# Performance work log

Hardware: AMD Instinct MI355X
Metric: run time of the kernel (lower is better)

## Reference

```python
import jax, jax.numpy as jnp
import numpy as np

EPS = 1e-7  # K.epsilon()
ROUTINGS = 3
NUM_CAPSULE = 8
FILTERS = 16


def squash(v, axis=-1):
    s2 = jnp.sum(jnp.square(v), axis=axis, keepdims=True)
    scale = s2 / (1.0 + s2) / jnp.sqrt(s2 + EPS)
    return scale * v


def _conv_per_caps(x, w):
    # x: [B,H,W,Cin], w: [k,k,Cin,Cout]
    return jax.lax.conv_general_dilated(
        x, w, window_strides=(1, 1), padding='SAME',
        dimension_numbers=('NHWC', 'HWIO', 'NHWC'))


def setup_inputs() -> dict:
    key = jax.random.key(0)
    k1, k2 = jax.random.split(key, 2)
    B, H, Wd, IN_CAPS, IN_F = 32, 32, 32, 8, 16
    input_tensor = jax.random.normal(k1, (B, H, Wd, IN_CAPS, IN_F), dtype=jnp.float32)
    # he_normal fan_in = k*k*Cin = 3*3*16 = 144
    W = jax.random.normal(k2, (IN_CAPS, 3, 3, IN_F, NUM_CAPSULE * FILTERS), dtype=jnp.float32) * np.sqrt(2.0 / 144.0)
    b = jnp.full((1, 1, NUM_CAPSULE, FILTERS), 0.1, dtype=jnp.float32)
    return {"input_tensor": input_tensor, "W": W, "b": b}


def reference(input_tensor, W, b):
    B, H, Wd, in_caps, in_f = input_tensor.shape
    # per-input-capsule conv: vmap over capsule axis of input and weight
    votes = jax.vmap(_conv_per_caps, in_axes=(3, 0), out_axes=1)(input_tensor, W)
    # [B, in_caps, H, W, num_cap*F] -> [B, in_caps, H, W, num_cap, F]
    votes = votes.reshape(B, in_caps, H, Wd, NUM_CAPSULE, FILTERS)

    # dynamic routing
    logits = jnp.zeros((B, in_caps, H, Wd, NUM_CAPSULE), dtype=votes.dtype)
    activation = None
    for i in range(ROUTINGS):
        route = jax.nn.softmax(logits, axis=-1)  # over output capsules
        # sum over input capsules of route-weighted votes, plus bias
        preactivate = jnp.einsum('bihwc,bihwcf->bhwcf', route, votes) + b
        activation = squash(preactivate, axis=-1)
        if i < ROUTINGS - 1:
            # scalar-product agreement
            logits = logits + jnp.einsum('bihwcf,bhwcf->bihwc', votes, activation)
    return activation.astype(jnp.float32)
```

## Files before the change

### kernel.cpp

```cpp
#include <hip/hip_runtime.h>
#include <math.h>


typedef _Float16 fp16x8 __attribute__((ext_vector_type(8)));
typedef float f32x4 __attribute__((ext_vector_type(4)));

#define EPS 1e-7f
constexpr int PSTRIDE = 136;
constexpr int LSTRIDE = 76;
constexpr int PXS     = 76;
constexpr int W_ELEMS = 40 * 8 * 64 * 8;

template<int CTRL>
__device__ __forceinline__ float dpp_rot(float v) {
    int s = __float_as_int(v);
    return __int_as_float(__builtin_amdgcn_update_dpp(s, s, CTRL, 0xF, 0xF, false));
}
__device__ __forceinline__ float sum16(float v) {
    v += dpp_rot<0x128>(v);
    v += dpp_rot<0x124>(v);
    v += dpp_rot<0x122>(v);
    v += dpp_rot<0x121>(v);
    return v;
}

__global__ __launch_bounds__(256)
void prep_weights(const float* __restrict__ wts,
                  _Float16* __restrict__ w16) {
    int n = blockIdx.x * 256 + threadIdx.x;
    if (n >= W_ELEMS) return;
    int j    = n & 7;
    int ln   = (n >> 3) & 63;
    int c0   = (n >> 9) & 7;
    int iq   = n >> 12;
    int i0   = iq / 5;
    int q0   = iq - i0 * 5;
    int quad0 = ln >> 4, fi0 = ln & 15;
    int k = q0 * 32 + quad0 * 8 + j;
    float w = 0.f;
    if (k < 144) w = wts[(i0 * 144 + k) * 128 + c0 * 16 + fi0];
    w16[n] = (_Float16)w;
}

__global__ __launch_bounds__(1024, 8)
void capsule_mfma_kernel(const float* __restrict__ x,
                         const _Float16* __restrict__ w16,
                         const float* __restrict__ bias,
                         float* __restrict__ out)
{
    __shared__ _Float16 patch[3 * 34 * PSTRIDE];
    __shared__ float lg_arr[32 * LSTRIDE];
    __shared__ float r_arr[32 * PXS];

    const int tid  = threadIdx.x;
    const int lane = tid & 63;
    const int wv   = tid >> 6;
    const int c    = wv & 7;
    const int Mt   = wv >> 3;
    const int fi   = lane & 15;
    const int quad = lane >> 4;
    const int lane8 = lane * 8;

    const int bid = blockIdx.x;
    const int h = bid & 31, b = bid >> 5;

    const float4* x4 = (const float4*)x;
    for (int idx = tid; idx < 102 * 32; idx += 1024) {
        int ch4  = idx & 31;
        int slot = idx >> 5;
        int row  = slot / 34;
        int colp = slot - row * 34;
        int gh = h - 1 + row;
        int gw = colp - 1;
        float4 v = {0.f, 0.f, 0.f, 0.f};
        if ((unsigned)gh < 32u && (unsigned)gw < 32u)
            v = x4[(((b * 32 + gh) * 32 + gw) << 5) + ch4];
        _Float16 ph[4];
        ph[0] = (_Float16)v.x; ph[1] = (_Float16)v.y;
        ph[2] = (_Float16)v.z; ph[3] = (_Float16)v.w;
        *(ushort4*)&patch[slot * PSTRIDE + ch4 * 4] = *(const ushort4*)ph;
    }
    __syncthreads();

    int a_off[5];
    #pragma unroll
    for (int q = 0; q < 5; ++q) {
        int tap = 2 * q + (quad >> 1);
        if (tap > 8) tap = 8;
        int dy = tap / 3, dx = tap - dy * 3;
        a_off[q] = (dy * 34 + (Mt * 16 + fi + dx)) * PSTRIDE + (quad & 1) * 8;
    }

    f32x4 acc[8];
    #pragma unroll
    for (int i = 0; i < 8; ++i) acc[i] = (f32x4){0.f, 0.f, 0.f, 0.f};

    #pragma unroll
    for (int q = 0; q < 5; ++q) {
        #pragma unroll
        for (int i = 0; i < 8; ++i) {
            int boff = ((i * 5 + q) * 8 + c) * 512 + lane8;
            fp16x8 bh = *(const fp16x8*)(w16 + boff);
            fp16x8 ah = *(const fp16x8*)(patch + a_off[q] + i * 16);
            acc[i] = __builtin_amdgcn_mfma_f32_16x16x32_f16(ah, bh, acc[i], 0, 0, 0);
        }
    }

    const float bb  = bias[c * 16 + fi];
    const int   px0 = Mt * 16 + quad * 4;
    float act[4];

    #pragma unroll
    for (int r = 0; r < 4; ++r) {
        float s = 0.f;
        #pragma unroll
        for (int i = 0; i < 8; ++i) s += acc[i][r];
        float pre = s * 0.125f + bb;
        float s2 = sum16(pre * pre);
        float scale = s2 * __builtin_amdgcn_rsqf(s2 + EPS) * __builtin_amdgcn_rcpf(1.f + s2);
        act[r] = scale * pre;
    }
    #pragma unroll
    for (int i = 0; i < 8; ++i)
        #pragma unroll
        for (int r = 0; r < 4; ++r) {
            float a = sum16(acc[i][r] * act[r]);
            if (fi == 0) lg_arr[(px0 + r) * LSTRIDE + i * 9 + c] = a;
        }
    __syncthreads();
    if (tid < 256) {
        int p = tid >> 3, ii = tid & 7;
        const float* lrow = &lg_arr[p * LSTRIDE + ii * 9];
        float m = lrow[0];
        #pragma unroll
        for (int cc = 1; cc < 8; ++cc) m = fmaxf(m, lrow[cc]);
        float e[8]; float den = 0.f;
        #pragma unroll
        for (int cc = 0; cc < 8; ++cc) { e[cc] = __expf(lrow[cc] - m); den += e[cc]; }
        float rd = __builtin_amdgcn_rcpf(den);
        #pragma unroll
        for (int cc = 0; cc < 8; ++cc) r_arr[p * PXS + cc * 8 + ii] = e[cc] * rd;
    }
    __syncthreads();

    #pragma unroll
    for (int r = 0; r < 4; ++r) {
        const float4* rp = (const float4*)&r_arr[(px0 + r) * PXS + c * 8];
        float4 r0 = rp[0], r1 = rp[1];
        float s;
        s  = r0.x * acc[0][r]; s = fmaf(r0.y, acc[1][r], s);
        s  = fmaf(r0.z, acc[2][r], s); s = fmaf(r0.w, acc[3][r], s);
        s  = fmaf(r1.x, acc[4][r], s); s = fmaf(r1.y, acc[5][r], s);
        s  = fmaf(r1.z, acc[6][r], s); s = fmaf(r1.w, acc[7][r], s);
        float pre = s + bb;
        float s2 = sum16(pre * pre);
        float scale = s2 * __builtin_amdgcn_rsqf(s2 + EPS) * __builtin_amdgcn_rcpf(1.f + s2);
        act[r] = scale * pre;
    }
    #pragma unroll
    for (int i = 0; i < 8; ++i)
        #pragma unroll
        for (int r = 0; r < 4; ++r) {
            float a = sum16(acc[i][r] * act[r]);
            if (fi == 0) lg_arr[(px0 + r) * LSTRIDE + i * 9 + c] += a;
        }
    __syncthreads();
    if (tid < 256) {
        int p = tid >> 3, ii = tid & 7;
        const float* lrow = &lg_arr[p * LSTRIDE + ii * 9];
        float m = lrow[0];
        #pragma unroll
        for (int cc = 1; cc < 8; ++cc) m = fmaxf(m, lrow[cc]);
        float e[8]; float den = 0.f;
        #pragma unroll
        for (int cc = 0; cc < 8; ++cc) { e[cc] = __expf(lrow[cc] - m); den += e[cc]; }
        float rd = __builtin_amdgcn_rcpf(den);
        #pragma unroll
        for (int cc = 0; cc < 8; ++cc) r_arr[p * PXS + cc * 8 + ii] = e[cc] * rd;
    }
    __syncthreads();

    #pragma unroll
    for (int r = 0; r < 4; ++r) {
        const float4* rp = (const float4*)&r_arr[(px0 + r) * PXS + c * 8];
        float4 r0 = rp[0], r1 = rp[1];
        float s;
        s  = r0.x * acc[0][r]; s = fmaf(r0.y, acc[1][r], s);
        s  = fmaf(r0.z, acc[2][r], s); s = fmaf(r0.w, acc[3][r], s);
        s  = fmaf(r1.x, acc[4][r], s); s = fmaf(r1.y, acc[5][r], s);
        s  = fmaf(r1.z, acc[6][r], s); s = fmaf(r1.w, acc[7][r], s);
        float pre = s + bb;
        float s2 = sum16(pre * pre);
        float scale = s2 * __builtin_amdgcn_rsqf(s2 + EPS) * __builtin_amdgcn_rcpf(1.f + s2);
        int px = px0 + r;
        out[(((b * 32 + h) * 32 + px) << 7) + c * 16 + fi] = scale * pre;
    }
}

extern "C" void kernel_launch(void* const* d_in, const int* in_sizes, int n_in,
                              void* d_out, int out_size, void* d_ws, size_t ws_size,
                              hipStream_t stream) {
    const float* x    = (const float*)d_in[0];
    const float* wts  = (const float*)d_in[1];
    const float* bias = (const float*)d_in[2];
    float* out        = (float*)d_out;
    _Float16* w16     = (_Float16*)d_ws;

    prep_weights<<<dim3(640), dim3(256), 0, stream>>>(wts, w16);
    capsule_mfma_kernel<<<dim3(1024), dim3(1024), 0, stream>>>(x, w16, bias, out);
}
```

Baseline: 118.2 us.

## Swap MFMA operands, drop weight prep kernel, use quad-shuffle reductions

Removes the separate fp16 weight-repacking launch and has each wave load fp32 weights straight from global memory, converting them to fp16 in registers. The weights become the A operand and the input patch the B operand, so each lane holds one pixel with four filter values. The 16-lane DPP reductions become two cross-quad shuffles, and output stores widen to float4. In exchange, every block does strided scalar global weight loads and conversions (8 loads per MFMA) instead of one contiguous 16-byte load.

```diff
diff --git a/kernel.cpp b/kernel.cpp
--- a/kernel.cpp
+++ b/kernel.cpp
@@ -9,42 +9,16 @@
 constexpr int PSTRIDE = 136;
 constexpr int LSTRIDE = 76;
 constexpr int PXS     = 76;
-constexpr int W_ELEMS = 40 * 8 * 64 * 8;
 
-template<int CTRL>
-__device__ __forceinline__ float dpp_rot(float v) {
-    int s = __float_as_int(v);
-    return __int_as_float(__builtin_amdgcn_update_dpp(s, s, CTRL, 0xF, 0xF, false));
-}
-__device__ __forceinline__ float sum16(float v) {
-    v += dpp_rot<0x128>(v);
-    v += dpp_rot<0x124>(v);
-    v += dpp_rot<0x122>(v);
-    v += dpp_rot<0x121>(v);
+__device__ __forceinline__ float sumquad(float v) {
+    v += __shfl_xor(v, 16);
+    v += __shfl_xor(v, 32);
     return v;
-}
-
-__global__ __launch_bounds__(256)
-void prep_weights(const float* __restrict__ wts,
-                  _Float16* __restrict__ w16) {
-    int n = blockIdx.x * 256 + threadIdx.x;
-    if (n >= W_ELEMS) return;
-    int j    = n & 7;
-    int ln   = (n >> 3) & 63;
-    int c0   = (n >> 9) & 7;
-    int iq   = n >> 12;
-    int i0   = iq / 5;
-    int q0   = iq - i0 * 5;
-    int quad0 = ln >> 4, fi0 = ln & 15;
-    int k = q0 * 32 + quad0 * 8 + j;
-    float w = 0.f;
-    if (k < 144) w = wts[(i0 * 144 + k) * 128 + c0 * 16 + fi0];
-    w16[n] = (_Float16)w;
 }
 
 __global__ __launch_bounds__(1024, 8)
 void capsule_mfma_kernel(const float* __restrict__ x,
-                         const _Float16* __restrict__ w16,
+                         const float* __restrict__ wts,
                          const float* __restrict__ bias,
                          float* __restrict__ out)
 {
@@ -57,9 +31,8 @@
     const int wv   = tid >> 6;
     const int c    = wv & 7;
     const int Mt   = wv >> 3;
-    const int fi   = lane & 15;
+    const int l15  = lane & 15;
     const int quad = lane >> 4;
-    const int lane8 = lane * 8;
 
     const int bid = blockIdx.x;
     const int h = bid & 31, b = bid >> 5;
@@ -88,45 +61,57 @@
         int tap = 2 * q + (quad >> 1);
         if (tap > 8) tap = 8;
         int dy = tap / 3, dx = tap - dy * 3;
-        a_off[q] = (dy * 34 + (Mt * 16 + fi + dx)) * PSTRIDE + (quad & 1) * 8;
+        a_off[q] = (dy * 34 + (Mt * 16 + l15 + dx)) * PSTRIDE + (quad & 1) * 8;
     }
 
     f32x4 acc[8];
     #pragma unroll
     for (int i = 0; i < 8; ++i) acc[i] = (f32x4){0.f, 0.f, 0.f, 0.f};
 
+    const float* wl = wts + quad * 8 * 128 + c * 16 + l15;
     #pragma unroll
     for (int q = 0; q < 5; ++q) {
         #pragma unroll
         for (int i = 0; i < 8; ++i) {
-            int boff = ((i * 5 + q) * 8 + c) * 512 + lane8;
-            fp16x8 bh = *(const fp16x8*)(w16 + boff);
-            fp16x8 ah = *(const fp16x8*)(patch + a_off[q] + i * 16);
-            acc[i] = __builtin_amdgcn_mfma_f32_16x16x32_f16(ah, bh, acc[i], 0, 0, 0);
+            const float* wp = wl + (i * 144 + q * 32) * 128;
+            union { fp16x8 v; _Float16 e[8]; } aw;
+            if (q < 4 || quad < 2) {
+                #pragma unroll
+                for (int j = 0; j < 8; ++j) aw.e[j] = (_Float16)wp[j * 128];
+            } else {
+                #pragma unroll
+                for (int j = 0; j < 8; ++j) aw.e[j] = (_Float16)0.f;
+            }
+            fp16x8 bh = *(const fp16x8*)(patch + a_off[q] + i * 16);
+            acc[i] = __builtin_amdgcn_mfma_f32_16x16x32_f16(aw.v, bh, acc[i], 0, 0, 0);
         }
     }
 
-    const float bb  = bias[c * 16 + fi];
-    const int   px0 = Mt * 16 + quad * 4;
-    float act[4];
+    const float4 bb4 = *(const float4*)(bias + c * 16 + quad * 4);
+    const float barr[4] = {bb4.x, bb4.y, bb4.z, bb4.w};
+    const int px = Mt * 16 + l15;
+
+    float pre[4], actv[4];
 
     #pragma unroll
     for (int r = 0; r < 4; ++r) {
-        float s = 0.f;
+        float s = acc[0][r] + acc[1][r] + acc[2][r] + acc[3][r]
+                + acc[4][r] + acc[5][r] + acc[6][r] + acc[7][r];
+        pre[r] = s * 0.125f + barr[r];
+    }
+    {
+        float s2 = sumquad(pre[0]*pre[0] + pre[1]*pre[1] + pre[2]*pre[2] + pre[3]*pre[3]);
+        float scale = s2 * __builtin_amdgcn_rsqf(s2 + EPS) * __builtin_amdgcn_rcpf(1.f + s2);
         #pragma unroll
-        for (int i = 0; i < 8; ++i) s += acc[i][r];
-        float pre = s * 0.125f + bb;
-        float s2 = sum16(pre * pre);
-        float scale = s2 * __builtin_amdgcn_rsqf(s2 + EPS) * __builtin_amdgcn_rcpf(1.f + s2);
-        act[r] = scale * pre;
+        for (int r = 0; r < 4; ++r) actv[r] = scale * pre[r];
     }
     #pragma unroll
-    for (int i = 0; i < 8; ++i)
-        #pragma unroll
-        for (int r = 0; r < 4; ++r) {
-            float a = sum16(acc[i][r] * act[r]);
-            if (fi == 0) lg_arr[(px0 + r) * LSTRIDE + i * 9 + c] = a;
-        }
+    for (int i = 0; i < 8; ++i) {
+        float t = acc[i][0]*actv[0] + acc[i][1]*actv[1]
+                + acc[i][2]*actv[2] + acc[i][3]*actv[3];
+        t = sumquad(t);
+        if (quad == 0) lg_arr[px * LSTRIDE + i * 9 + c] = t;
+    }
     __syncthreads();
     if (tid < 256) {
         int p = tid >> 3, ii = tid & 7;
@@ -143,27 +128,30 @@
     }
     __syncthreads();
 
-    #pragma unroll
-    for (int r = 0; r < 4; ++r) {
-        const float4* rp = (const float4*)&r_arr[(px0 + r) * PXS + c * 8];
+    {
+        const float4* rp = (const float4*)&r_arr[px * PXS + c * 8];
         float4 r0 = rp[0], r1 = rp[1];
-        float s;
-        s  = r0.x * acc[0][r]; s = fmaf(r0.y, acc[1][r], s);
-        s  = fmaf(r0.z, acc[2][r], s); s = fmaf(r0.w, acc[3][r], s);
-        s  = fmaf(r1.x, acc[4][r], s); s = fmaf(r1.y, acc[5][r], s);
-        s  = fmaf(r1.z, acc[6][r], s); s = fmaf(r1.w, acc[7][r], s);
-        float pre = s + bb;
-        float s2 = sum16(pre * pre);
+        #pragma unroll
+        for (int r = 0; r < 4; ++r) {
+            float s;
+            s  = r0.x * acc[0][r]; s = fmaf(r0.y, acc[1][r], s);
+            s  = fmaf(r0.z, acc[2][r], s); s = fmaf(r0.w, acc[3][r], s);
+            s  = fmaf(r1.x, acc[4][r], s); s = fmaf(r1.y, acc[5][r], s);
+            s  = fmaf(r1.z, acc[6][r], s); s = fmaf(r1.w, acc[7][r], s);
+            pre[r] = s + barr[r];
+        }
+        float s2 = sumquad(pre[0]*pre[0] + pre[1]*pre[1] + pre[2]*pre[2] + pre[3]*pre[3]);
         float scale = s2 * __builtin_amdgcn_rsqf(s2 + EPS) * __builtin_amdgcn_rcpf(1.f + s2);
-        act[r] = scale * pre;
+        #pragma unroll
+        for (int r = 0; r < 4; ++r) actv[r] = scale * pre[r];
     }
     #pragma unroll
-    for (int i = 0; i < 8; ++i)
-        #pragma unroll
-        for (int r = 0; r < 4; ++r) {
-            float a = sum16(acc[i][r] * act[r]);
-            if (fi == 0) lg_arr[(px0 + r) * LSTRIDE + i * 9 + c] += a;
-        }
+    for (int i = 0; i < 8; ++i) {
+        float t = acc[i][0]*actv[0] + acc[i][1]*actv[1]
+                + acc[i][2]*actv[2] + acc[i][3]*actv[3];
+        t = sumquad(t);
+        if (quad == 0) lg_arr[px * LSTRIDE + i * 9 + c] += t;
+    }
     __syncthreads();
     if (tid < 256) {
         int p = tid >> 3, ii = tid & 7;
@@ -180,20 +168,22 @@
     }
     __syncthreads();
 
-    #pragma unroll
-    for (int r = 0; r < 4; ++r) {
-        const float4* rp = (const float4*)&r_arr[(px0 + r) * PXS + c * 8];
+    {
+        const float4* rp = (const float4*)&r_arr[px * PXS + c * 8];
         float4 r0 = rp[0], r1 = rp[1];
-        float s;
-        s  = r0.x * acc[0][r]; s = fmaf(r0.y, acc[1][r], s);
-        s  = fmaf(r0.z, acc[2][r], s); s = fmaf(r0.w, acc[3][r], s);
-        s  = fmaf(r1.x, acc[4][r], s); s = fmaf(r1.y, acc[5][r], s);
-        s  = fmaf(r1.z, acc[6][r], s); s = fmaf(r1.w, acc[7][r], s);
-        float pre = s + bb;
-        float s2 = sum16(pre * pre);
+        #pragma unroll
+        for (int r = 0; r < 4; ++r) {
+            float s;
+            s  = r0.x * acc[0][r]; s = fmaf(r0.y, acc[1][r], s);
+            s  = fmaf(r0.z, acc[2][r], s); s = fmaf(r0.w, acc[3][r], s);
+            s  = fmaf(r1.x, acc[4][r], s); s = fmaf(r1.y, acc[5][r], s);
+            s  = fmaf(r1.z, acc[6][r], s); s = fmaf(r1.w, acc[7][r], s);
+            pre[r] = s + barr[r];
+        }
+        float s2 = sumquad(pre[0]*pre[0] + pre[1]*pre[1] + pre[2]*pre[2] + pre[3]*pre[3]);
         float scale = s2 * __builtin_amdgcn_rsqf(s2 + EPS) * __builtin_amdgcn_rcpf(1.f + s2);
-        int px = px0 + r;
-        out[(((b * 32 + h) * 32 + px) << 7) + c * 16 + fi] = scale * pre;
+        float4 o4 = { scale*pre[0], scale*pre[1], scale*pre[2], scale*pre[3] };
+        *(float4*)(out + (((b * 32 + h) * 32 + px) << 7) + c * 16 + quad * 4) = o4;
     }
 }
 
@@ -204,8 +194,6 @@
     const float* wts  = (const float*)d_in[1];
     const float* bias = (const float*)d_in[2];
     float* out        = (float*)d_out;
-    _Float16* w16     = (_Float16*)d_ws;
 
-    prep_weights<<<dim3(640), dim3(256), 0, stream>>>(wts, w16);
-    capsule_mfma_kernel<<<dim3(1024), dim3(1024), 0, stream>>>(x, w16, bias, out);
+    capsule_mfma_kernel<<<dim3(1024), dim3(1024), 0, stream>>>(x, wts, bias, out);
 }
```

Result: slower. 137.5 us (+16.3%).
